# Kernel tuning notes

Hardware: AMD Instinct MI355X
Metric: run time of the kernel (lower is better)

## Reference

```python
import jax, jax.numpy as jnp
import numpy as np

E = 8            # num_local_experts
K = 2            # top-2 gate
CAP_FACTOR = 1.0 # tutel default capacity factor


def setup_inputs() -> dict:
    key = jax.random.key(0)
    k0, k1, k2, k3 = jax.random.split(key, 4)
    B, N, D, H = 8, 8192, 512, 512
    s = 0.02
    return {
        "x": jax.random.normal(k0, (B, N, D), jnp.float32),
        "Wg": jax.random.normal(k1, (D, E), jnp.float32) * s,
        "W1": jax.random.normal(k2, (E, D, H), jnp.float32) * s,
        "b1": jnp.zeros((E, H), jnp.float32),
        "W2": jax.random.normal(k3, (E, H, D), jnp.float32) * s,
        "b2": jnp.zeros((E, D), jnp.float32),
    }


def _moe(x, Wg, W1, b1, W2, b2):
    B, N, D = x.shape
    T = B * N
    xt = x.reshape(T, D)
    # --- gating (Top2Gate): softmax over experts, take top-2, renormalize ---
    gates = jax.nn.softmax(xt @ Wg, axis=-1)            # [T, E]
    topw, topi = jax.lax.top_k(gates, K)                # [T, K]
    topw = topw / jnp.sum(topw, axis=-1, keepdims=True)
    # --- capacity & per-expert positions (k=0 assignments fill first) ---
    C = int(np.ceil(K * T / E * CAP_FACTOR))
    onehot = jax.nn.one_hot(topi, E, dtype=jnp.int32)   # [T, K, E]
    flat = onehot.transpose(1, 0, 2).reshape(K * T, E)  # k-major order
    pos_flat = jnp.cumsum(flat, axis=0) - 1             # running count per expert
    pos = (pos_flat * flat).sum(-1).reshape(K, T).T     # [T, K] slot within expert
    keep = (pos < C).astype(xt.dtype)                   # [T, K] capacity drop mask
    # --- dispatch: scatter tokens into [E, C, D] expert buffers ---
    ei = topi.reshape(-1)                               # [T*K]
    pi = jnp.clip(pos, 0, C - 1).reshape(-1)            # [T*K]
    vals = (xt[:, None, :] * keep[:, :, None]).reshape(T * K, D)
    buf = jnp.zeros((E, C, D), xt.dtype).at[ei, pi].add(vals)
    # --- per-expert FFN (identity activation) ---
    h = jnp.einsum('ecd,edh->ech', buf, W1) + b1[:, None, :]
    out = jnp.einsum('ech,ehd->ecd', h, W2) + b2[:, None, :]
    # --- combine: gather expert outputs, weight, sum over k ---
    gathered = out[ei, pi].reshape(T, K, D)
    y = jnp.sum(gathered * (topw * keep)[:, :, None], axis=1)
    return y.reshape(B, N, D)


def reference(x, Wg, W1, b1, W2, b2):
    y = _moe(x, Wg, W1, b1, W2, b2)        # [B, N, D]
    return jax.nn.log_softmax(jnp.sum(y, axis=2), axis=1)  # [B, N]
```

## Files before the change

### kernel.cpp

```cpp
#include <hip/hip_runtime.h>

#define T_TOK 65536
#define DDIM 512
#define NEXP 8
#define CAP 16384

__device__ inline float wave_sum(float v) {
#pragma unroll
  for (int m = 1; m < 64; m <<= 1) v += __shfl_xor(v, m, 64);
  return v;
}

template <int CTRL>
__device__ __forceinline__ float dppf(float v) {
  return __int_as_float(
      __builtin_amdgcn_mov_dpp(__float_as_int(v), CTRL, 0xf, 0xf, true));
}
__device__ __forceinline__ void pl32swap(float& a, float& b) {
  asm("v_permlane32_swap_b32 %0, %1" : "+v"(a), "+v"(b));
}
__device__ __forceinline__ void pl16swap(float& a, float& b) {
  asm("v_permlane16_swap_b32 %0, %1" : "+v"(a), "+v"(b));
}

__global__ void k_w2s(const float* __restrict__ W2, const float* __restrict__ Wg,
                      float* __restrict__ w2s, float* __restrict__ wT) {
  if (blockIdx.x < 1024) {
    int w = threadIdx.x >> 6, lane = threadIdx.x & 63;
    int row = blockIdx.x * 4 + w;
    const float* p = W2 + (size_t)row * 512;
    float sum = 0.f;
#pragma unroll
    for (int j = 0; j < 8; ++j) sum += p[lane + j * 64];
    sum = wave_sum(sum);
    if (lane == 0) w2s[row] = sum;
  } else {
    int i = (blockIdx.x - 1024) * 256 + threadIdx.x;
    int e = i >> 9, d = i & 511;
    wT[i] = Wg[d * 8 + e];
  }
}

__global__ void k_v_beta(const float* __restrict__ W1, const float* __restrict__ b1,
                         const float* __restrict__ b2, const float* __restrict__ w2s,
                         float* __restrict__ wT, float* __restrict__ beta) {
  int w = threadIdx.x >> 6, lane = threadIdx.x & 63;
  if (blockIdx.x < 1024) {
    int rid = blockIdx.x * 4 + w;
    int e = rid >> 9, d = rid & 511;
    const float* p = W1 + (size_t)rid * 512;
    const float* q = w2s + e * 512;
    float sum = 0.f;
#pragma unroll
    for (int j = 0; j < 8; ++j) { int h = lane + j * 64; sum += p[h] * q[h]; }
    sum = wave_sum(sum);
    if (lane == 0) wT[(size_t)(8 + e) * 512 + d] = sum;
  } else {
#pragma unroll
    for (int r = 0; r < 2; ++r) {
      int e = w + r * 4;
      float sum = 0.f;
#pragma unroll
      for (int j = 0; j < 8; ++j) {
        int i = lane + j * 64;
        sum += b1[e * 512 + i] * w2s[e * 512 + i] + b2[e * 512 + i];
      }
      sum = wave_sum(sum);
      if (lane == 0) beta[e] = sum;
    }
  }
}

__global__ __launch_bounds__(256, 4) void k_dots(const float* __restrict__ x,
                                                 const float* __restrict__ wT,
                                                 float* __restrict__ dots) {
  const int lane = threadIdx.x & 63;
  const int wave = threadIdx.x >> 6;
  const int wo = wave & 1;
  const int tset = wave >> 1;
  const int tbase = blockIdx.x * 64 + tset * 32;

  float w[8][8];
#pragma unroll
  for (int o = 0; o < 8; ++o) {
    const float* wp = wT + (size_t)(wo * 8 + o) * 512 + 8 * lane;
    float4 wa = *reinterpret_cast<const float4*>(wp);
    float4 wb = *reinterpret_cast<const float4*>(wp + 4);
    w[o][0] = wa.x; w[o][1] = wa.y; w[o][2] = wa.z; w[o][3] = wa.w;
    w[o][4] = wb.x; w[o][5] = wb.y; w[o][6] = wb.z; w[o][7] = wb.w;
  }

  const bool kb3 = (lane & 8) != 0;
  const float* xb = x + (size_t)tbase * 512 + 8 * lane;

  auto proc = [&](int tok, float4 x0, float4 x1) {
    float p[8];
#pragma unroll
    for (int o = 0; o < 8; ++o)
      p[o] = x0.x * w[o][0] + x0.y * w[o][1] + x0.z * w[o][2] + x0.w * w[o][3] +
             x1.x * w[o][4] + x1.y * w[o][5] + x1.z * w[o][6] + x1.w * w[o][7];
    float a[4];
#pragma unroll
    for (int j = 0; j < 4; ++j) {
      float u = p[j], v = p[j + 4];
      pl32swap(u, v);
      a[j] = u + v;
    }
    float b[2];
#pragma unroll
    for (int j = 0; j < 2; ++j) {
      float u = a[j], v = a[j + 2];
      pl16swap(u, v);
      b[j] = u + v;
    }
    float snd = kb3 ? b[0] : b[1];
    float kp  = kb3 ? b[1] : b[0];
    float c = kp + dppf<0x128>(snd);
    c += dppf<0x141>(c);
    c += dppf<0x4E>(c);
    c += dppf<0xB1>(c);
    if ((lane & 7) == 0)
      dots[(size_t)tok * 16 + wo * 8 + (lane >> 3)] = c;
  };

  float4 s00, s01, s10, s11, s20, s21, s30, s31;
  const float* q;
  q = xb;              s00 = *reinterpret_cast<const float4*>(q); s01 = *reinterpret_cast<const float4*>(q + 4);
  q = xb + 512;        s10 = *reinterpret_cast<const float4*>(q); s11 = *reinterpret_cast<const float4*>(q + 4);
  q = xb + 1024;       s20 = *reinterpret_cast<const float4*>(q); s21 = *reinterpret_cast<const float4*>(q + 4);

#pragma unroll
  for (int r = 0; r < 32; r += 4) {
    q = xb + (size_t)(r + 3) * 512;
    s30 = *reinterpret_cast<const float4*>(q); s31 = *reinterpret_cast<const float4*>(q + 4);
    proc(tbase + r, s00, s01);
    if (r + 4 < 32) {
      q = xb + (size_t)(r + 4) * 512;
      s00 = *reinterpret_cast<const float4*>(q); s01 = *reinterpret_cast<const float4*>(q + 4);
    }
    proc(tbase + r + 1, s10, s11);
    if (r + 5 < 32) {
      q = xb + (size_t)(r + 5) * 512;
      s10 = *reinterpret_cast<const float4*>(q); s11 = *reinterpret_cast<const float4*>(q + 4);
    }
    proc(tbase + r + 2, s20, s21);
    if (r + 6 < 32) {
      q = xb + (size_t)(r + 6) * 512;
      s20 = *reinterpret_cast<const float4*>(q); s21 = *reinterpret_cast<const float4*>(q + 4);
    }
    proc(tbase + r + 3, s30, s31);
  }
}

__global__ void k_top2(const float* __restrict__ dots, const float* __restrict__ beta,
                       float4* __restrict__ wd, int* __restrict__ epk,
                       int* __restrict__ hist) {
  __shared__ int c0[8], c1[8];
  int tid = threadIdx.x;
  if (tid < 8) { c0[tid] = 0; c1[tid] = 0; }
  __syncthreads();
  int t = blockIdx.x * 256 + tid;
  const float* p = dots + (size_t)t * 16;
  float l[8], dv[8];
#pragma unroll
  for (int e = 0; e < 8; ++e) { l[e] = p[e]; dv[e] = p[8 + e]; }
  int e1 = 0; float v1 = l[0];
#pragma unroll
  for (int e = 1; e < 8; ++e) if (l[e] > v1) { v1 = l[e]; e1 = e; }
  int e2 = 0; float v2 = -3.4e38f;
#pragma unroll
  for (int e = 0; e < 8; ++e) if (e != e1 && l[e] > v2) { v2 = l[e]; e2 = e; }
  float wexp = expf(v2 - v1);
  float w1 = 1.f / (1.f + wexp);
  float w2 = wexp * w1;
  float d1 = 0.f, d2 = 0.f;
#pragma unroll
  for (int e = 0; e < 8; ++e) {
    d1 = (e == e1) ? dv[e] : d1;
    d2 = (e == e2) ? dv[e] : d2;
  }
  float4 o; o.x = w1; o.y = w2; o.z = d1 + beta[e1]; o.w = d2 + beta[e2];
  wd[t] = o;
  epk[t] = e1 | (e2 << 8);
  atomicAdd(&c0[e1], 1);
  atomicAdd(&c1[e2], 1);
  __syncthreads();
  if (tid < 8) {
    hist[blockIdx.x * 8 + tid] = c0[tid];
    hist[(256 + blockIdx.x) * 8 + tid] = c1[tid];
  }
}

__global__ __launch_bounds__(512) void k_scan(const int* __restrict__ hist,
                                              int* __restrict__ off) {
  __shared__ int sH[4096];
  __shared__ int sT[512];
  int tid = threadIdx.x;
#pragma unroll
  for (int i = tid; i < 4096; i += 512) sH[i] = hist[i];
  __syncthreads();
  int e = tid & 7, g = tid >> 3;
  int run = 0;
#pragma unroll
  for (int i = g * 8; i < g * 8 + 8; ++i) {
    int cv = sH[i * 8 + e]; sH[i * 8 + e] = run; run += cv;
  }
  sT[tid] = run;
  __syncthreads();
  int inc = run;
#pragma unroll
  for (int st = 1; st < 64; st <<= 1) {
    int add = (g >= st) ? sT[tid - st * 8] : 0;
    __syncthreads();
    inc += add;
    sT[tid] = inc;
    __syncthreads();
  }
  int exc = inc - run;
#pragma unroll
  for (int i = g * 8; i < g * 8 + 8; ++i) sH[i * 8 + e] += exc;
  __syncthreads();
#pragma unroll
  for (int i = tid; i < 4096; i += 512) off[i] = sH[i];
}

__global__ void k_keep(const int* __restrict__ epk, const float4* __restrict__ wd,
                       const int* __restrict__ off, float* __restrict__ s) {
  __shared__ int sC0[32], sC1[32];
  int tid = threadIdx.x, lane = tid & 63, w = tid >> 6;
  int t = blockIdx.x * 256 + tid;
  int ep = epk[t]; int e1 = ep & 255, e2 = ep >> 8;
  unsigned long long lt = (1ull << lane) - 1ull;
  int wr0 = 0, wr1 = 0;
#pragma unroll
  for (int e = 0; e < 8; ++e) {
    unsigned long long m0 = __ballot(e1 == e);
    unsigned long long m1 = __ballot(e2 == e);
    if (e == e1) wr0 = __popcll(m0 & lt);
    if (e == e2) wr1 = __popcll(m1 & lt);
    if (lane == 0) { sC0[w * 8 + e] = __popcll(m0); sC1[w * 8 + e] = __popcll(m1); }
  }
  __syncthreads();
  int woff0 = 0, woff1 = 0;
  for (int wp = 0; wp < 4; ++wp) {
    if (wp < w) { woff0 += sC0[wp * 8 + e1]; woff1 += sC1[wp * 8 + e2]; }
  }
  int b = blockIdx.x;
  int pos0 = off[b * 8 + e1] + woff0 + wr0;
  int pos1 = off[(256 + b) * 8 + e2] + woff1 + wr1;
  float4 v = wd[t];
  float sv = 0.f;
  if (pos0 < CAP) sv += v.x * v.z;
  if (pos1 < CAP) sv += v.y * v.w;
  s[t] = sv;
}

__global__ __launch_bounds__(1024) void k_lsm(const float* __restrict__ s,
                                              float* __restrict__ out) {
  __shared__ float sRa[16], sRb[16];
  int tid = threadIdx.x, lane = tid & 63, w = tid >> 6;
  size_t base = (size_t)blockIdx.x * 8192;
  float v[8];
#pragma unroll
  for (int j = 0; j < 8; ++j) v[j] = s[base + tid + j * 1024];
  float mx = v[0];
#pragma unroll
  for (int j = 1; j < 8; ++j) mx = fmaxf(mx, v[j]);
#pragma unroll
  for (int m = 1; m < 64; m <<= 1) mx = fmaxf(mx, __shfl_xor(mx, m, 64));
  if (lane == 0) sRa[w] = mx;
  __syncthreads();
#pragma unroll
  for (int i = 0; i < 16; ++i) mx = fmaxf(mx, sRa[i]);
  float sum = 0.f;
#pragma unroll
  for (int j = 0; j < 8; ++j) sum += expf(v[j] - mx);
#pragma unroll
  for (int m = 1; m < 64; m <<= 1) sum += __shfl_xor(sum, m, 64);
  if (lane == 0) sRb[w] = sum;
  __syncthreads();
  float tot = 0.f;
#pragma unroll
  for (int i = 0; i < 16; ++i) tot += sRb[i];
  float lse = logf(tot);
#pragma unroll
  for (int j = 0; j < 8; ++j) out[base + tid + j * 1024] = v[j] - mx - lse;
}

extern "C" void kernel_launch(void* const* d_in, const int* in_sizes, int n_in,
                              void* d_out, int out_size, void* d_ws, size_t ws_size,
                              hipStream_t stream) {
  const float* x  = (const float*)d_in[0];
  const float* Wg = (const float*)d_in[1];
  const float* W1 = (const float*)d_in[2];
  const float* b1 = (const float*)d_in[3];
  const float* W2 = (const float*)d_in[4];
  const float* b2 = (const float*)d_in[5];
  float* out = (float*)d_out;
  char* ws = (char*)d_ws;

  float*  w2s  = (float*)(ws);
  float*  wT   = (float*)(ws + (16u << 10));
  float*  beta = (float*)(ws + (48u << 10));
  float*  dots = (float*)(ws + (64u << 10));
  char*   p1   = ws + (64u << 10) + (4u << 20);
  float4* wd   = (float4*)(p1);
  int*    epk  = (int*)(p1 + (1u << 20));
  int*    hist = (int*)(p1 + (1u << 20) + (256u << 10));
  int*    offa = (int*)(p1 + (1u << 20) + (272u << 10));
  float*  s    = (float*)(p1 + (1u << 20) + (288u << 10));

  hipLaunchKernelGGL(k_w2s,    dim3(1040), dim3(256),  0, stream, W2, Wg, w2s, wT);
  hipLaunchKernelGGL(k_v_beta, dim3(1025), dim3(256),  0, stream, W1, b1, b2, w2s, wT, beta);
  hipLaunchKernelGGL(k_dots,   dim3(1024), dim3(256),  0, stream, x, wT, dots);
  hipLaunchKernelGGL(k_top2,   dim3(256),  dim3(256),  0, stream, dots, beta, wd, epk, hist);
  hipLaunchKernelGGL(k_scan,   dim3(1),    dim3(512),  0, stream, hist, offa);
  hipLaunchKernelGGL(k_keep,   dim3(256),  dim3(256),  0, stream, epk, wd, offa, s);
  hipLaunchKernelGGL(k_lsm,    dim3(8),    dim3(1024), 0, stream, s, out);
}
```

Baseline: 51.52 us.

## Fuse top-2 gating into the dots kernel via shared memory

Merges k_top2 into k_dots. Each 1024-thread block computes 256 tokens' 16 dot values into padded shared memory, then its first 256 threads do the top-2 selection, weights and histogram. This drops the 4 MB dots round trip through global memory and one kernel launch. In exchange the block grows to 1024 threads and the grid shrinks to 256 blocks, which may reduce latency hiding and leaves 3/4 of the threads idle during the top-2 phase.

```diff
diff --git a/kernel.cpp b/kernel.cpp
--- a/kernel.cpp
+++ b/kernel.cpp
@@ -71,14 +71,20 @@
   }
 }
 
-__global__ __launch_bounds__(256, 4) void k_dots(const float* __restrict__ x,
-                                                 const float* __restrict__ wT,
-                                                 float* __restrict__ dots) {
-  const int lane = threadIdx.x & 63;
-  const int wave = threadIdx.x >> 6;
+__global__ __launch_bounds__(1024, 4) void k_dots(const float* __restrict__ x,
+                                                  const float* __restrict__ wT,
+                                                  const float* __restrict__ beta,
+                                                  float4* __restrict__ wd,
+                                                  int* __restrict__ epk,
+                                                  int* __restrict__ hist) {
+  __shared__ float sD[256 * 17];
+  __shared__ int c0[8], c1[8];
+  const int tid = threadIdx.x;
+  const int lane = tid & 63;
+  const int wave = tid >> 6;
   const int wo = wave & 1;
   const int tset = wave >> 1;
-  const int tbase = blockIdx.x * 64 + tset * 32;
+  const int tbase = blockIdx.x * 256 + tset * 32;
 
   float w[8][8];
 #pragma unroll
@@ -93,7 +99,7 @@
   const bool kb3 = (lane & 8) != 0;
   const float* xb = x + (size_t)tbase * 512 + 8 * lane;
 
-  auto proc = [&](int tok, float4 x0, float4 x1) {
+  auto proc = [&](int r, float4 x0, float4 x1) {
     float p[8];
 #pragma unroll
     for (int o = 0; o < 8; ++o)
@@ -120,70 +126,66 @@
     c += dppf<0x4E>(c);
     c += dppf<0xB1>(c);
     if ((lane & 7) == 0)
-      dots[(size_t)tok * 16 + wo * 8 + (lane >> 3)] = c;
+      sD[(tset * 32 + r) * 17 + wo * 8 + (lane >> 3)] = c;
   };
 
   float4 s00, s01, s10, s11, s20, s21, s30, s31;
   const float* q;
-  q = xb;              s00 = *reinterpret_cast<const float4*>(q); s01 = *reinterpret_cast<const float4*>(q + 4);
-  q = xb + 512;        s10 = *reinterpret_cast<const float4*>(q); s11 = *reinterpret_cast<const float4*>(q + 4);
-  q = xb + 1024;       s20 = *reinterpret_cast<const float4*>(q); s21 = *reinterpret_cast<const float4*>(q + 4);
+  q = xb;        s00 = *reinterpret_cast<const float4*>(q); s01 = *reinterpret_cast<const float4*>(q + 4);
+  q = xb + 512;  s10 = *reinterpret_cast<const float4*>(q); s11 = *reinterpret_cast<const float4*>(q + 4);
+  q = xb + 1024; s20 = *reinterpret_cast<const float4*>(q); s21 = *reinterpret_cast<const float4*>(q + 4);
 
 #pragma unroll
   for (int r = 0; r < 32; r += 4) {
     q = xb + (size_t)(r + 3) * 512;
     s30 = *reinterpret_cast<const float4*>(q); s31 = *reinterpret_cast<const float4*>(q + 4);
-    proc(tbase + r, s00, s01);
+    proc(r, s00, s01);
     if (r + 4 < 32) {
       q = xb + (size_t)(r + 4) * 512;
       s00 = *reinterpret_cast<const float4*>(q); s01 = *reinterpret_cast<const float4*>(q + 4);
     }
-    proc(tbase + r + 1, s10, s11);
+    proc(r + 1, s10, s11);
     if (r + 5 < 32) {
       q = xb + (size_t)(r + 5) * 512;
       s10 = *reinterpret_cast<const float4*>(q); s11 = *reinterpret_cast<const float4*>(q + 4);
     }
-    proc(tbase + r + 2, s20, s21);
+    proc(r + 2, s20, s21);
     if (r + 6 < 32) {
       q = xb + (size_t)(r + 6) * 512;
       s20 = *reinterpret_cast<const float4*>(q); s21 = *reinterpret_cast<const float4*>(q + 4);
     }
-    proc(tbase + r + 3, s30, s31);
-  }
-}
-
-__global__ void k_top2(const float* __restrict__ dots, const float* __restrict__ beta,
-                       float4* __restrict__ wd, int* __restrict__ epk,
-                       int* __restrict__ hist) {
-  __shared__ int c0[8], c1[8];
-  int tid = threadIdx.x;
+    proc(r + 3, s30, s31);
+  }
+
+  __syncthreads();
   if (tid < 8) { c0[tid] = 0; c1[tid] = 0; }
   __syncthreads();
-  int t = blockIdx.x * 256 + tid;
-  const float* p = dots + (size_t)t * 16;
-  float l[8], dv[8];
-#pragma unroll
-  for (int e = 0; e < 8; ++e) { l[e] = p[e]; dv[e] = p[8 + e]; }
-  int e1 = 0; float v1 = l[0];
-#pragma unroll
-  for (int e = 1; e < 8; ++e) if (l[e] > v1) { v1 = l[e]; e1 = e; }
-  int e2 = 0; float v2 = -3.4e38f;
-#pragma unroll
-  for (int e = 0; e < 8; ++e) if (e != e1 && l[e] > v2) { v2 = l[e]; e2 = e; }
-  float wexp = expf(v2 - v1);
-  float w1 = 1.f / (1.f + wexp);
-  float w2 = wexp * w1;
-  float d1 = 0.f, d2 = 0.f;
-#pragma unroll
-  for (int e = 0; e < 8; ++e) {
-    d1 = (e == e1) ? dv[e] : d1;
-    d2 = (e == e2) ? dv[e] : d2;
-  }
-  float4 o; o.x = w1; o.y = w2; o.z = d1 + beta[e1]; o.w = d2 + beta[e2];
-  wd[t] = o;
-  epk[t] = e1 | (e2 << 8);
-  atomicAdd(&c0[e1], 1);
-  atomicAdd(&c1[e2], 1);
+  if (tid < 256) {
+    const int t = blockIdx.x * 256 + tid;
+    float l[8], dv[8];
+#pragma unroll
+    for (int e = 0; e < 8; ++e) { l[e] = sD[tid * 17 + e]; dv[e] = sD[tid * 17 + 8 + e]; }
+    int e1 = 0; float v1 = l[0];
+#pragma unroll
+    for (int e = 1; e < 8; ++e) if (l[e] > v1) { v1 = l[e]; e1 = e; }
+    int e2 = 0; float v2 = -3.4e38f;
+#pragma unroll
+    for (int e = 0; e < 8; ++e) if (e != e1 && l[e] > v2) { v2 = l[e]; e2 = e; }
+    float wexp = expf(v2 - v1);
+    float w1 = 1.f / (1.f + wexp);
+    float w2 = wexp * w1;
+    float d1 = 0.f, d2 = 0.f;
+#pragma unroll
+    for (int e = 0; e < 8; ++e) {
+      d1 = (e == e1) ? dv[e] : d1;
+      d2 = (e == e2) ? dv[e] : d2;
+    }
+    float4 o; o.x = w1; o.y = w2; o.z = d1 + beta[e1]; o.w = d2 + beta[e2];
+    wd[t] = o;
+    epk[t] = e1 | (e2 << 8);
+    atomicAdd(&c0[e1], 1);
+    atomicAdd(&c1[e2], 1);
+  }
   __syncthreads();
   if (tid < 8) {
     hist[blockIdx.x * 8 + tid] = c0[tid];
@@ -302,18 +304,15 @@
   float*  w2s  = (float*)(ws);
   float*  wT   = (float*)(ws + (16u << 10));
   float*  beta = (float*)(ws + (48u << 10));
-  float*  dots = (float*)(ws + (64u << 10));
-  char*   p1   = ws + (64u << 10) + (4u << 20);
-  float4* wd   = (float4*)(p1);
-  int*    epk  = (int*)(p1 + (1u << 20));
-  int*    hist = (int*)(p1 + (1u << 20) + (256u << 10));
-  int*    offa = (int*)(p1 + (1u << 20) + (272u << 10));
-  float*  s    = (float*)(p1 + (1u << 20) + (288u << 10));
+  float4* wd   = (float4*)(ws + (64u << 10));
+  int*    epk  = (int*)(ws + (64u << 10) + (1u << 20));
+  int*    hist = (int*)(ws + (64u << 10) + (1u << 20) + (256u << 10));
+  int*    offa = (int*)(ws + (64u << 10) + (1u << 20) + (272u << 10));
+  float*  s    = (float*)(ws + (64u << 10) + (1u << 20) + (288u << 10));
 
   hipLaunchKernelGGL(k_w2s,    dim3(1040), dim3(256),  0, stream, W2, Wg, w2s, wT);
   hipLaunchKernelGGL(k_v_beta, dim3(1025), dim3(256),  0, stream, W1, b1, b2, w2s, wT, beta);
-  hipLaunchKernelGGL(k_dots,   dim3(1024), dim3(256),  0, stream, x, wT, dots);
-  hipLaunchKernelGGL(k_top2,   dim3(256),  dim3(256),  0, stream, dots, beta, wd, epk, hist);
+  hipLaunchKernelGGL(k_dots,   dim3(256),  dim3(1024), 0, stream, x, wT, beta, wd, epk, hist);
   hipLaunchKernelGGL(k_scan,   dim3(1),    dim3(512),  0, stream, hist, offa);
   hipLaunchKernelGGL(k_keep,   dim3(256),  dim3(256),  0, stream, epk, wd, offa, s);
   hipLaunchKernelGGL(k_lsm,    dim3(8),    dim3(1024), 0, stream, s, out);
```

Measured after the change: 48.88 us (median of 2 runs). 5.1% less time.
